# Optimization experiments

Hardware: AMD Instinct MI355X
Metric: run time of the kernel (lower is better)

The kernel has to match this reference:

```python
import jax, jax.numpy as jnp
import numpy as np

K_S = 7
PAD = 3

def _normalize(x, eps=1e-7):
    n = jnp.sqrt(jnp.sum(x * x, axis=-1, keepdims=True))
    return x / jnp.maximum(n, eps)

def _sample_early(feat, pid):
    # feat: [B,C,H,W]; gather fixed random patch ids shared across batch
    B, C, H, W = feat.shape
    fr = jnp.transpose(feat, (0, 2, 3, 1)).reshape(B, H * W, C)
    x = fr[:, pid, :].reshape(B * pid.shape[0], C)
    return _normalize(x)

def _qs_attn(feat, num_patches):
    B, C, H, W = feat.shape
    L = H * W
    fr = jnp.transpose(feat, (0, 2, 3, 1)).reshape(B, L, C)  # [B,L,C]
    # F.unfold(kernel=7, stride=1, padding=3): torch layout [B, C*49, L] (channel-major)
    pad = jnp.pad(feat, ((0, 0), (0, 0), (PAD, PAD), (PAD, PAD)))
    patches = jnp.stack([pad[:, :, i:i + H, j:j + W]
                         for i in range(K_S) for j in range(K_S)], axis=2)  # [B,C,49,H,W]
    feat_local = patches.reshape(B, C * K_S * K_S, L)
    # faithful to original: permute then reshape (B, L, k*k, C)
    feat_k_local = jnp.transpose(feat_local, (0, 2, 1)).reshape(B, L, K_S * K_S, C)
    # local attention: dots over window, softmax over the 49 window positions
    dots_local = jnp.einsum('blkc,blc->blk', feat_k_local, fr)
    attn_local = jax.nn.softmax(dots_local, axis=2)  # [B,L,49]
    logp = jnp.log(attn_local)
    prob = jnp.where(jnp.isinf(logp), 0.0, -logp)
    entropy = jnp.sum(attn_local * prob, axis=2)  # [B,L]
    idx = jnp.argsort(entropy, axis=1)[:, :num_patches]  # lowest-entropy patches [B,P]
    # global attention, only rows at selected patch ids (same math as slicing full BxLxL)
    q = jnp.take_along_axis(fr, idx[:, :, None], axis=1)  # [B,P,C]
    dots_global = jnp.einsum('bpc,blc->bpl', q, fr)
    attn_qs = jax.nn.softmax(dots_global, axis=2)  # [B,P,L]
    out = jnp.einsum('bpl,blc->bpc', attn_qs, fr)  # [B,P,C]
    return _normalize(out.reshape(B * num_patches, C))

def setup_inputs() -> dict:
    key = jax.random.key(0)
    k0, k1, k2, k3, k4, k5, k6 = jax.random.split(key, 7)
    return {
        'feat0': jax.random.normal(k0, (2, 64, 256, 256), dtype=jnp.float32),
        'feat1': jax.random.normal(k1, (2, 128, 128, 128), dtype=jnp.float32),
        'feat2': jax.random.normal(k2, (2, 256, 64, 64), dtype=jnp.float32),
        'feat3': jax.random.normal(k3, (2, 256, 64, 64), dtype=jnp.float32),
        'pid0': jax.random.randint(k4, (64,), 0, 256 * 256, dtype=jnp.int64)
                if jax.config.jax_enable_x64 else jax.random.randint(k4, (64,), 0, 256 * 256),
        'pid1': jax.random.randint(k5, (64,), 0, 128 * 128),
        'pid2': jax.random.randint(k6, (64,), 0, 64 * 64),
        'num_patches': 64,
    }

def reference(feat0, feat1, feat2, feat3, pid0, pid1, pid2, num_patches):
    x0 = _sample_early(feat0, pid0)
    x1 = _sample_early(feat1, pid1)
    x2 = _sample_early(feat2, pid2)
    x3 = _qs_attn(feat3, num_patches)
    return (x0, x1, x2, x3)
```

## Files before the change

kernel.cpp:

```cpp
#include <hip/hip_runtime.h>
#include <hip/hip_bf16.h>
#include <cstdint>
#include <cstddef>

__device__ __forceinline__ float wave_max_f(float v){
  #pragma unroll
  for (int m = 32; m; m >>= 1) v = fmaxf(v, __shfl_xor(v, m));
  return v;
}
__device__ __forceinline__ float wave_sum_f(float v){
  #pragma unroll
  for (int m = 32; m; m >>= 1) v += __shfl_xor(v, m);
  return v;
}
__device__ __forceinline__ int wave_sum_i(int v){
  #pragma unroll
  for (int m = 32; m; m >>= 1) v += __shfl_xor(v, m);
  return v;
}

#define C3   256
#define HW3  4096
#define NP   64

template<int C, int LOGHW>
__device__ __forceinline__ void sample_body(const float* __restrict__ feat,
                                            const int* __restrict__ pid,
                                            float* __restrict__ out,
                                            int r, int lane){
  const int b = r >> 6, p = r & 63;
  const int l = pid[p];
  const float* fb = feat + (((size_t)b * C) << LOGHW);
  constexpr int V = C / 64;
  float v[V];
  float sq = 0.f;
  #pragma unroll
  for (int i = 0; i < V; ++i){
    const int c = lane + 64 * i;
    v[i] = fb[(((size_t)c) << LOGHW) + l];
    sq += v[i] * v[i];
  }
  sq = wave_sum_f(sq);
  const float nrm = fmaxf(sqrtf(sq), 1e-7f);
  #pragma unroll
  for (int i = 0; i < V; ++i)
    out[(size_t)r * C + lane + 64 * i] = v[i] / nrm;
}

__global__ __launch_bounds__(1024, 8)
void ldots_kernel(const float* __restrict__ feat3, float* __restrict__ dotsl,
                  const float* __restrict__ f0, const float* __restrict__ f1,
                  const float* __restrict__ f2,
                  const int* __restrict__ p0, const int* __restrict__ p1,
                  const int* __restrict__ p2,
                  float* __restrict__ o0, float* __restrict__ o1,
                  float* __restrict__ o2){
  __shared__ float fr_sh[C3 * 64];
  const int raw = blockIdx.x;
  const int tid = threadIdx.x, wid = tid >> 6, lane = tid & 63;

  if (raw >= 512){
    const int sidx = ((raw - 512) << 4) | wid;
    const int g = sidx >> 7, r = sidx & 127;
    if (g == 0)      sample_body<64, 16>(f0, p0, o0, r, lane);
    else if (g == 1) sample_body<128, 14>(f1, p1, o1, r, lane);
    else             sample_body<256, 12>(f2, p2, o2, r, lane);
    return;
  }

  const int work = (raw & 7) * 64 + (raw >> 3);
  const int kg = work & 3;
  const int bh = work >> 2;
  const int b = bh >> 6, h = bh & 63;
  const int w = lane;
  const float* fb = feat3 + ((size_t)b << 20);

  {
    const int c2b = wid << 4;
    #pragma unroll
    for (int j = 0; j < 16; ++j){
      const int c2 = c2b + j;
      fr_sh[(c2 << 6) + w] = fb[((size_t)c2 << 12) + (h << 6) + w];
    }
  }
  __syncthreads();

  const int k2v = (wid << 2) | kg;
  if (k2v >= 49) return;
  const int k2 = __builtin_amdgcn_readfirstlane(k2v);
  const float* fr_w = fr_sh + w;
  const int f0i = k2 << 8;
  const int c0 = f0i / 49;
  const int k0 = f0i - c0 * 49;

  int   vof[7];
  float msk[7];
  #pragma unroll
  for (int kj = 0; kj < 7; ++kj){
    const int s = w + kj - 3;
    msk[kj] = ((unsigned)s < 64u) ? 1.f : 0.f;
    vof[kj] = s < 0 ? 0 : (s > 63 ? 63 : s);
  }

  float acc = 0.f;
  int c2 = 0;

  auto partial = [&](int c, int klo, int khi){
    for (int k = klo; k < khi; ++k){
      const int ki = k / 7, kj = k - (k / 7) * 7;
      const int hh = h + ki - 3;
      float wv = 0.f;
      if ((unsigned)hh < 64u){
        const int sw = w + kj - 3;
        const int swc = sw < 0 ? 0 : (sw > 63 ? 63 : sw);
        const float x = fb[((size_t)c << 12) + (hh << 6) + swc];
        wv = ((unsigned)sw < 64u) ? x : 0.f;
      }
      acc = fmaf(wv, fr_w[c2 << 6], acc);
      ++c2;
    }
  };

  partial(c0, k0, 49);

  #pragma unroll
  for (int j = 1; j <= 4; ++j){
    const int c = c0 + j;
    const float* chan = fb + ((size_t)c << 12);
    #pragma unroll
    for (int ki = 0; ki < 7; ++ki){
      const int hh = h + ki - 3;
      if ((unsigned)hh < 64u){
        const float* row = chan + (hh << 6);
        #pragma unroll
        for (int kj = 0; kj < 7; ++kj){
          const float x = row[vof[kj]];
          acc = fmaf(x * msk[kj], fr_w[(c2 + ki * 7 + kj) << 6], acc);
        }
      }
    }
    c2 += 49;
  }

  {
    const int rem = 11 + k0;
    const int khi = rem < 49 ? rem : 49;
    partial(c0 + 5, 0, khi);
    if (rem > 49) partial(c0 + 6, 0, rem - 49);
  }

  dotsl[(((size_t)(b * 49 + k2)) << 12) + (h << 6) + w] = acc;
}

__global__ __launch_bounds__(64)
void lent_kernel(const float* __restrict__ dotsl, float* __restrict__ ent){
  const int blk = blockIdx.x;
  const int b = blk >> 6;
  const int l = ((blk & 63) << 6) + threadIdx.x;
  const float* dl = dotsl + (((size_t)b * 49) << 12);
  float m = -INFINITY;
  #pragma unroll
  for (int k = 0; k < 49; ++k) m = fmaxf(m, dl[((size_t)k << 12) + l]);
  float s = 0.f, ts = 0.f;
  #pragma unroll
  for (int k = 0; k < 49; ++k){
    const float d = dl[((size_t)k << 12) + l] - m;
    const float e = expf(d);
    s += e; ts += e * d;
  }
  ent[b * HW3 + l] = logf(s) - ts / s;
}

__global__ __launch_bounds__(256)
void rank_select_kernel(const float* __restrict__ ent, int* __restrict__ idx){
  __shared__ unsigned long long keys[HW3];
  const int blk = blockIdx.x;
  const int b  = blk >> 6;
  const int cg = blk & 63;
  const int t = threadIdx.x, wid = t >> 6, lane = t & 63;
  for (int i = t; i < HW3; i += 256){
    const float e = ent[b * HW3 + i];
    unsigned u = __float_as_uint(e);
    u = (u & 0x80000000u) ? ~u : (u | 0x80000000u);
    keys[i] = ((unsigned long long)u << 32) | (unsigned)i;
  }
  __syncthreads();
  #pragma unroll
  for (int j = 0; j < 16; ++j){
    const int cand = (cg << 6) + (wid << 4) + j;
    const unsigned long long kc = keys[cand];
    int cnt = 0;
    #pragma unroll 8
    for (int i = lane; i < HW3; i += 64)
      cnt += (keys[i] < kc) ? 1 : 0;
    cnt = wave_sum_i(cnt);
    if (lane == 0 && cnt < NP) idx[b * NP + cnt] = cand;
  }
}

__global__ __launch_bounds__(256)
void gdots_kernel(const float* __restrict__ feat3, const int* __restrict__ idx,
                  float* __restrict__ dg, float* __restrict__ bmax){
  __shared__ float4 q_int[C3];
  __shared__ float red4[4][4];
  const int raw = blockIdx.x;
  const int work = (raw & 7) * 64 + (raw >> 3);
  const int bpg = work >> 4, lc = work & 15;
  const int b = bpg >> 4;
  const int bp0 = (b << 6) + ((bpg & 15) << 2);
  const int t = threadIdx.x, lane = t & 63, wid = t >> 6;
  const float* fb = feat3 + ((size_t)b << 20);
  {
    float4 qv;
    qv.x = fb[((size_t)t << 12) + idx[bp0 + 0]];
    qv.y = fb[((size_t)t << 12) + idx[bp0 + 1]];
    qv.z = fb[((size_t)t << 12) + idx[bp0 + 2]];
    qv.w = fb[((size_t)t << 12) + idx[bp0 + 3]];
    q_int[t] = qv;
  }
  __syncthreads();
  const int l = (lc << 8) + t;
  float a0 = 0.f, a1 = 0.f, a2 = 0.f, a3 = 0.f;
  #pragma unroll 8
  for (int c = 0; c < C3; ++c){
    const float fv = fb[((size_t)c << 12) + l];
    const float4 q = q_int[c];
    a0 = fmaf(fv, q.x, a0); a1 = fmaf(fv, q.y, a1);
    a2 = fmaf(fv, q.z, a2); a3 = fmaf(fv, q.w, a3);
  }
  dg[((size_t)(bp0 + 0) << 12) + l] = a0;
  dg[((size_t)(bp0 + 1) << 12) + l] = a1;
  dg[((size_t)(bp0 + 2) << 12) + l] = a2;
  dg[((size_t)(bp0 + 3) << 12) + l] = a3;
  const float m0 = wave_max_f(a0), m1 = wave_max_f(a1);
  const float m2 = wave_max_f(a2), m3 = wave_max_f(a3);
  if (lane == 0){
    red4[wid][0] = m0; red4[wid][1] = m1;
    red4[wid][2] = m2; red4[wid][3] = m3;
  }
  __syncthreads();
  if (t < 4){
    const float m = fmaxf(fmaxf(red4[0][t], red4[1][t]),
                          fmaxf(red4[2][t], red4[3][t]));
    bmax[(bp0 + t) * 16 + lc] = m;
  }
}

#define PSW(l) ((l) ^ (((l) >> 3) & 7))
__global__ __launch_bounds__(256)
void pv_kernel(const float* __restrict__ feat3, const float* __restrict__ dg,
               const float* __restrict__ bmax, float* __restrict__ outraw){
  __shared__ float4 p_int[HW3];
  float* red = reinterpret_cast<float*>(p_int);
  const int raw = blockIdx.x;
  const int work = (raw & 7) * 32 + (raw >> 3);
  const int bpg = work >> 3, cg = work & 7;
  const int b = bpg >> 4;
  const int bp0 = (b << 6) + ((bpg & 15) << 2);
  const int t = threadIdx.x, lane = t & 63, wid = t >> 6;
  const float* fb = feat3 + ((size_t)b << 20);

  float e_reg[4][16];
  float iq[4];
  #pragma unroll
  for (int q = 0; q < 4; ++q){
    const int bp = bp0 + q;
    float m = -INFINITY;
    #pragma unroll
    for (int i = 0; i < 16; ++i) m = fmaxf(m, bmax[bp * 16 + i]);
    float s = 0.f;
    #pragma unroll
    for (int i = 0; i < 16; ++i){
      const float e = expf(dg[((size_t)bp << 12) + (i << 8) + t] - m);
      e_reg[q][i] = e;
      s += e;
    }
    s = wave_sum_f(s);
    if (lane == 0) red[wid] = s;
    __syncthreads();
    const float stot = red[0] + red[1] + red[2] + red[3];
    __syncthreads();
    iq[q] = 1.f / stot;
  }

  #pragma unroll
  for (int i = 0; i < 16; ++i){
    const int l = (i << 8) + t;
    float4 pv;
    pv.x = e_reg[0][i] * iq[0];
    pv.y = e_reg[1][i] * iq[1];
    pv.z = e_reg[2][i] * iq[2];
    pv.w = e_reg[3][i] * iq[3];
    p_int[PSW(l)] = pv;
  }
  __syncthreads();
  float s[8][4];
  #pragma unroll
  for (int j = 0; j < 8; ++j)
    #pragma unroll
    for (int q = 0; q < 4; ++q) s[j][q] = 0.f;

  const int cbase = (cg << 5) + (wid << 3);
  for (int i = 0; i < 16; ++i){
    const int l4 = (i << 6) + lane;
    const float4 p0 = p_int[PSW(4 * l4 + 0)];
    const float4 p1 = p_int[PSW(4 * l4 + 1)];
    const float4 p2 = p_int[PSW(4 * l4 + 2)];
    const float4 p3 = p_int[PSW(4 * l4 + 3)];
    #pragma unroll
    for (int j = 0; j < 8; ++j){
      const float4 a = *reinterpret_cast<const float4*>(
          fb + (((size_t)(cbase + j)) << 12) + 4 * (size_t)l4);
      s[j][0] += a.x * p0.x + a.y * p1.x + a.z * p2.x + a.w * p3.x;
      s[j][1] += a.x * p0.y + a.y * p1.y + a.z * p2.y + a.w * p3.y;
      s[j][2] += a.x * p0.z + a.y * p1.z + a.z * p2.z + a.w * p3.z;
      s[j][3] += a.x * p0.w + a.y * p1.w + a.z * p2.w + a.w * p3.w;
    }
  }
  #pragma unroll
  for (int j = 0; j < 8; ++j){
    #pragma unroll
    for (int q = 0; q < 4; ++q){
      const float v = wave_sum_f(s[j][q]);
      if (lane == 0) outraw[(bp0 + q) * C3 + cbase + j] = v;
    }
  }
}

__global__ __launch_bounds__(256)
void norm_kernel(const float* __restrict__ outraw, float* __restrict__ out3){
  __shared__ float red[4];
  const int bp = blockIdx.x, t = threadIdx.x, lane = t & 63, wid = t >> 6;
  const float v = outraw[bp * C3 + t];
  const float sq = wave_sum_f(v * v);
  if (lane == 0) red[wid] = sq;
  __syncthreads();
  const float nrm = fmaxf(sqrtf(red[0] + red[1] + red[2] + red[3]), 1e-7f);
  out3[(size_t)bp * C3 + t] = v / nrm;
}

extern "C" void kernel_launch(void* const* d_in, const int* in_sizes, int n_in,
                              void* d_out, int out_size, void* d_ws, size_t ws_size,
                              hipStream_t stream){
  const float* feat0 = (const float*)d_in[0];
  const float* feat1 = (const float*)d_in[1];
  const float* feat2 = (const float*)d_in[2];
  const float* feat3 = (const float*)d_in[3];
  const int*   pid0  = (const int*)d_in[4];
  const int*   pid1  = (const int*)d_in[5];
  const int*   pid2  = (const int*)d_in[6];

  float* out  = (float*)d_out;
  float* out0 = out;
  float* out1 = out + 8192;
  float* out2 = out + 24576;
  float* out3 = out + 57344;

  float* ws       = (float*)d_ws;
  float* ent_ws   = ws;
  int*   idx_ws   = (int*)(ws + 8192);
  float* dotsl_ws = ws + 8320;
  float* dg_ws    = dotsl_ws + 401408;
  float* bmax_ws  = dg_ws + 524288;
  float* oraw_ws  = bmax_ws + 2048;

  ldots_kernel<<<536, 1024, 0, stream>>>(feat3, dotsl_ws,
                                         feat0, feat1, feat2,
                                         pid0, pid1, pid2,
                                         out0, out1, out2);
  lent_kernel<<<128, 64, 0, stream>>>(dotsl_ws, ent_ws);
  rank_select_kernel<<<128, 256, 0, stream>>>(ent_ws, idx_ws);
  gdots_kernel<<<512, 256, 0, stream>>>(feat3, idx_ws, dg_ws, bmax_ws);
  pv_kernel<<<256, 256, 0, stream>>>(feat3, dg_ws, bmax_ws, oraw_ws);
  norm_kernel<<<128, 256, 0, stream>>>(oraw_ws, out3);
}
```

Baseline: 98.57 us.

## Split PV over L into 8 slices with separate softmax-stats kernel

Softmax row max and inverse sum move into a new gsm_kernel. pv_kernel now splits the L dimension into 8 slices, so it launches 2048 blocks instead of 256, and each block builds only a small slice of probabilities in shared memory. Partial outputs are written per slice and summed in norm_kernel. This raises parallelism and lowers shared memory per block to improve occupancy, at the cost of one extra launch, recomputing exp across channel groups, and reusing workspace regions.

Measured after the change: 138.2 us. 40.2% more time.

```diff
diff --git a/kernel.cpp b/kernel.cpp
--- a/kernel.cpp
+++ b/kernel.cpp
@@ -246,54 +246,60 @@
   }
 }
 
-#define PSW(l) ((l) ^ (((l) >> 3) & 7))
 __global__ __launch_bounds__(256)
+void gsm_kernel(const float* __restrict__ dg, const float* __restrict__ bmax,
+                float* __restrict__ mrow, float* __restrict__ srow){
+  __shared__ float red[4];
+  const int bp = blockIdx.x, t = threadIdx.x, lane = t & 63, wid = t >> 6;
+  float m = -INFINITY;
+  #pragma unroll
+  for (int i = 0; i < 16; ++i) m = fmaxf(m, bmax[bp * 16 + i]);
+  float s = 0.f;
+  #pragma unroll
+  for (int i = 0; i < 16; ++i) s += expf(dg[((size_t)bp << 12) + (i << 8) + t] - m);
+  s = wave_sum_f(s);
+  if (lane == 0) red[wid] = s;
+  __syncthreads();
+  if (t == 0){
+    mrow[bp] = m;
+    srow[bp] = 1.f / (red[0] + red[1] + red[2] + red[3]);
+  }
+}
+
+__global__ __launch_bounds__(256, 6)
 void pv_kernel(const float* __restrict__ feat3, const float* __restrict__ dg,
-               const float* __restrict__ bmax, float* __restrict__ outraw){
-  __shared__ float4 p_int[HW3];
-  float* red = reinterpret_cast<float*>(p_int);
+               const float* __restrict__ mrow, const float* __restrict__ srow,
+               float* __restrict__ opart){
+  __shared__ float4 pp[4][130];
   const int raw = blockIdx.x;
-  const int work = (raw & 7) * 32 + (raw >> 3);
-  const int bpg = work >> 3, cg = work & 7;
-  const int b = bpg >> 4;
-  const int bp0 = (b << 6) + ((bpg & 15) << 2);
+  const int work = (raw & 7) * 256 + (raw >> 3);
+  const int pg = work & 15;
+  const int rest = work >> 4;
+  const int ls = rest & 7;
+  const int cg = (rest >> 3) & 7;
+  const int b  = rest >> 6;
+  const int bp0 = (b << 6) + (pg << 2);
   const int t = threadIdx.x, lane = t & 63, wid = t >> 6;
   const float* fb = feat3 + ((size_t)b << 20);
 
-  float e_reg[4][16];
-  float iq[4];
-  #pragma unroll
-  for (int q = 0; q < 4; ++q){
-    const int bp = bp0 + q;
-    float m = -INFINITY;
-    #pragma unroll
-    for (int i = 0; i < 16; ++i) m = fmaxf(m, bmax[bp * 16 + i]);
-    float s = 0.f;
-    #pragma unroll
-    for (int i = 0; i < 16; ++i){
-      const float e = expf(dg[((size_t)bp << 12) + (i << 8) + t] - m);
-      e_reg[q][i] = e;
-      s += e;
-    }
-    s = wave_sum_f(s);
-    if (lane == 0) red[wid] = s;
-    __syncthreads();
-    const float stot = red[0] + red[1] + red[2] + red[3];
-    __syncthreads();
-    iq[q] = 1.f / stot;
-  }
-
-  #pragma unroll
-  for (int i = 0; i < 16; ++i){
-    const int l = (i << 8) + t;
+  const float m0 = mrow[bp0 + 0], i0 = srow[bp0 + 0];
+  const float m1 = mrow[bp0 + 1], i1 = srow[bp0 + 1];
+  const float m2 = mrow[bp0 + 2], i2 = srow[bp0 + 2];
+  const float m3 = mrow[bp0 + 3], i3 = srow[bp0 + 3];
+
+  #pragma unroll
+  for (int rep = 0; rep < 2; ++rep){
+    const int lo = t + (rep << 8);
+    const int l = (ls << 9) + lo;
     float4 pv;
-    pv.x = e_reg[0][i] * iq[0];
-    pv.y = e_reg[1][i] * iq[1];
-    pv.z = e_reg[2][i] * iq[2];
-    pv.w = e_reg[3][i] * iq[3];
-    p_int[PSW(l)] = pv;
-  }
-  __syncthreads();
+    pv.x = expf(dg[((size_t)(bp0 + 0) << 12) + l] - m0) * i0;
+    pv.y = expf(dg[((size_t)(bp0 + 1) << 12) + l] - m1) * i1;
+    pv.z = expf(dg[((size_t)(bp0 + 2) << 12) + l] - m2) * i2;
+    pv.w = expf(dg[((size_t)(bp0 + 3) << 12) + l] - m3) * i3;
+    pp[lo & 3][lo >> 2] = pv;
+  }
+  __syncthreads();
+
   float s[8][4];
   #pragma unroll
   for (int j = 0; j < 8; ++j)
@@ -301,16 +307,17 @@
     for (int q = 0; q < 4; ++q) s[j][q] = 0.f;
 
   const int cbase = (cg << 5) + (wid << 3);
-  for (int i = 0; i < 16; ++i){
-    const int l4 = (i << 6) + lane;
-    const float4 p0 = p_int[PSW(4 * l4 + 0)];
-    const float4 p1 = p_int[PSW(4 * l4 + 1)];
-    const float4 p2 = p_int[PSW(4 * l4 + 2)];
-    const float4 p3 = p_int[PSW(4 * l4 + 3)];
+  #pragma unroll
+  for (int ii = 0; ii < 2; ++ii){
+    const int l4 = (ii << 6) + lane;
+    const float4 p0 = pp[0][l4];
+    const float4 p1 = pp[1][l4];
+    const float4 p2 = pp[2][l4];
+    const float4 p3 = pp[3][l4];
     #pragma unroll
     for (int j = 0; j < 8; ++j){
       const float4 a = *reinterpret_cast<const float4*>(
-          fb + (((size_t)(cbase + j)) << 12) + 4 * (size_t)l4);
+          fb + (((size_t)(cbase + j)) << 12) + (ls << 9) + 4 * (size_t)l4);
       s[j][0] += a.x * p0.x + a.y * p1.x + a.z * p2.x + a.w * p3.x;
       s[j][1] += a.x * p0.y + a.y * p1.y + a.z * p2.y + a.w * p3.y;
       s[j][2] += a.x * p0.z + a.y * p1.z + a.z * p2.z + a.w * p3.z;
@@ -322,16 +329,20 @@
     #pragma unroll
     for (int q = 0; q < 4; ++q){
       const float v = wave_sum_f(s[j][q]);
-      if (lane == 0) outraw[(bp0 + q) * C3 + cbase + j] = v;
+      if (lane == 0)
+        opart[((((bp0 + q) << 8) | (cbase + j)) << 3) | ls] = v;
     }
   }
 }
 
 __global__ __launch_bounds__(256)
-void norm_kernel(const float* __restrict__ outraw, float* __restrict__ out3){
+void norm_kernel(const float* __restrict__ opart, float* __restrict__ out3){
   __shared__ float red[4];
   const int bp = blockIdx.x, t = threadIdx.x, lane = t & 63, wid = t >> 6;
-  const float v = outraw[bp * C3 + t];
+  const float* op = opart + (((size_t)(bp << 8) | t) << 3);
+  float v = 0.f;
+  #pragma unroll
+  for (int ls = 0; ls < 8; ++ls) v += op[ls];
   const float sq = wave_sum_f(v * v);
   if (lane == 0) red[wid] = sq;
   __syncthreads();
@@ -362,7 +373,9 @@
   float* dotsl_ws = ws + 8320;
   float* dg_ws    = dotsl_ws + 401408;
   float* bmax_ws  = dg_ws + 524288;
-  float* oraw_ws  = bmax_ws + 2048;
+  float* mrow_ws  = ent_ws;
+  float* srow_ws  = ent_ws + 128;
+  float* opart_ws = dotsl_ws;
 
   ldots_kernel<<<536, 1024, 0, stream>>>(feat3, dotsl_ws,
                                          feat0, feat1, feat2,
@@ -371,6 +384,7 @@
   lent_kernel<<<128, 64, 0, stream>>>(dotsl_ws, ent_ws);
   rank_select_kernel<<<128, 256, 0, stream>>>(ent_ws, idx_ws);
   gdots_kernel<<<512, 256, 0, stream>>>(feat3, idx_ws, dg_ws, bmax_ws);
-  pv_kernel<<<256, 256, 0, stream>>>(feat3, dg_ws, bmax_ws, oraw_ws);
-  norm_kernel<<<128, 256, 0, stream>>>(oraw_ws, out3);
-}
+  gsm_kernel<<<128, 256, 0, stream>>>(dg_ws, bmax_ws, mrow_ws, srow_ws);
+  pv_kernel<<<2048, 256, 0, stream>>>(feat3, dg_ws, mrow_ws, srow_ws, opart_ws);
+  norm_kernel<<<128, 256, 0, stream>>>(opart_ws, out3);
+}
```

## Split softmax normalization into separate kernel and read probabilities from global in PV

Applied to the files above, without the earlier changes.

Moves the softmax exp/normalize of the global attention rows out of pv_kernel into a new pfill_kernel that writes normalized probabilities back in place. Each pv block previously recomputed the softmax for its 4 rows, redundantly across 8 channel groups, then staged the result in 64KB of LDS. Now pv_kernel reads probabilities directly from global/L2 with no LDS, which permits higher occupancy (launch bounds 6) and a work order grouping channel groups. This adds an extra kernel launch and a global round trip for the probabilities.

After: 125.4 us. 1.27x slower.

```diff
diff --git a/kernel.cpp b/kernel.cpp
--- a/kernel.cpp
+++ b/kernel.cpp
@@ -246,83 +246,75 @@
   }
 }
 
-#define PSW(l) ((l) ^ (((l) >> 3) & 7))
 __global__ __launch_bounds__(256)
-void pv_kernel(const float* __restrict__ feat3, const float* __restrict__ dg,
-               const float* __restrict__ bmax, float* __restrict__ outraw){
-  __shared__ float4 p_int[HW3];
-  float* red = reinterpret_cast<float*>(p_int);
+void pfill_kernel(float* __restrict__ dg, const float* __restrict__ bmax){
+  __shared__ float red[4];
+  const int bp = blockIdx.x, t = threadIdx.x, lane = t & 63, wid = t >> 6;
+  float m = -INFINITY;
+  #pragma unroll
+  for (int i = 0; i < 16; ++i) m = fmaxf(m, bmax[bp * 16 + i]);
+  float e[16];
+  float s = 0.f;
+  #pragma unroll
+  for (int i = 0; i < 16; ++i){
+    e[i] = expf(dg[((size_t)bp << 12) + (i << 8) + t] - m);
+    s += e[i];
+  }
+  s = wave_sum_f(s);
+  if (lane == 0) red[wid] = s;
+  __syncthreads();
+  const float inv = 1.f / (red[0] + red[1] + red[2] + red[3]);
+  #pragma unroll
+  for (int i = 0; i < 16; ++i)
+    dg[((size_t)bp << 12) + (i << 8) + t] = e[i] * inv;
+}
+
+__global__ __launch_bounds__(256, 6)
+void pv_kernel(const float* __restrict__ feat3, const float* __restrict__ p,
+               float* __restrict__ outraw){
   const int raw = blockIdx.x;
   const int work = (raw & 7) * 32 + (raw >> 3);
-  const int bpg = work >> 3, cg = work & 7;
-  const int b = bpg >> 4;
-  const int bp0 = (b << 6) + ((bpg & 15) << 2);
+  const int cg = work >> 5;
+  const int rest = work & 31;
+  const int b = rest >> 4, pg = rest & 15;
+  const int bp0 = (b << 6) + (pg << 2);
   const int t = threadIdx.x, lane = t & 63, wid = t >> 6;
   const float* fb = feat3 + ((size_t)b << 20);
-
-  float e_reg[4][16];
-  float iq[4];
-  #pragma unroll
-  for (int q = 0; q < 4; ++q){
-    const int bp = bp0 + q;
-    float m = -INFINITY;
-    #pragma unroll
-    for (int i = 0; i < 16; ++i) m = fmaxf(m, bmax[bp * 16 + i]);
-    float s = 0.f;
-    #pragma unroll
-    for (int i = 0; i < 16; ++i){
-      const float e = expf(dg[((size_t)bp << 12) + (i << 8) + t] - m);
-      e_reg[q][i] = e;
-      s += e;
-    }
-    s = wave_sum_f(s);
-    if (lane == 0) red[wid] = s;
-    __syncthreads();
-    const float stot = red[0] + red[1] + red[2] + red[3];
-    __syncthreads();
-    iq[q] = 1.f / stot;
-  }
-
-  #pragma unroll
-  for (int i = 0; i < 16; ++i){
-    const int l = (i << 8) + t;
-    float4 pv;
-    pv.x = e_reg[0][i] * iq[0];
-    pv.y = e_reg[1][i] * iq[1];
-    pv.z = e_reg[2][i] * iq[2];
-    pv.w = e_reg[3][i] * iq[3];
-    p_int[PSW(l)] = pv;
-  }
-  __syncthreads();
-  float s[8][4];
+  const int c0 = (cg << 5) + (wid << 3);
+
+  const float4* p0 = reinterpret_cast<const float4*>(p + ((size_t)(bp0 + 0) << 12));
+  const float4* p1 = reinterpret_cast<const float4*>(p + ((size_t)(bp0 + 1) << 12));
+  const float4* p2 = reinterpret_cast<const float4*>(p + ((size_t)(bp0 + 2) << 12));
+  const float4* p3 = reinterpret_cast<const float4*>(p + ((size_t)(bp0 + 3) << 12));
+
+  float acc[8][4];
   #pragma unroll
   for (int j = 0; j < 8; ++j)
     #pragma unroll
-    for (int q = 0; q < 4; ++q) s[j][q] = 0.f;
-
-  const int cbase = (cg << 5) + (wid << 3);
-  for (int i = 0; i < 16; ++i){
-    const int l4 = (i << 6) + lane;
-    const float4 p0 = p_int[PSW(4 * l4 + 0)];
-    const float4 p1 = p_int[PSW(4 * l4 + 1)];
-    const float4 p2 = p_int[PSW(4 * l4 + 2)];
-    const float4 p3 = p_int[PSW(4 * l4 + 3)];
+    for (int q = 0; q < 4; ++q) acc[j][q] = 0.f;
+
+  for (int ii = 0; ii < 16; ++ii){
+    const int l4 = (ii << 6) + lane;
+    const float4 q0 = p0[l4];
+    const float4 q1 = p1[l4];
+    const float4 q2 = p2[l4];
+    const float4 q3 = p3[l4];
     #pragma unroll
     for (int j = 0; j < 8; ++j){
       const float4 a = *reinterpret_cast<const float4*>(
-          fb + (((size_t)(cbase + j)) << 12) + 4 * (size_t)l4);
-      s[j][0] += a.x * p0.x + a.y * p1.x + a.z * p2.x + a.w * p3.x;
-      s[j][1] += a.x * p0.y + a.y * p1.y + a.z * p2.y + a.w * p3.y;
-      s[j][2] += a.x * p0.z + a.y * p1.z + a.z * p2.z + a.w * p3.z;
-      s[j][3] += a.x * p0.w + a.y * p1.w + a.z * p2.w + a.w * p3.w;
+          fb + (((size_t)(c0 + j)) << 12) + 4 * (size_t)l4);
+      acc[j][0] += a.x * q0.x + a.y * q0.y + a.z * q0.z + a.w * q0.w;
+      acc[j][1] += a.x * q1.x + a.y * q1.y + a.z * q1.z + a.w * q1.w;
+      acc[j][2] += a.x * q2.x + a.y * q2.y + a.z * q2.z + a.w * q2.w;
+      acc[j][3] += a.x * q3.x + a.y * q3.y + a.z * q3.z + a.w * q3.w;
     }
   }
   #pragma unroll
   for (int j = 0; j < 8; ++j){
     #pragma unroll
     for (int q = 0; q < 4; ++q){
-      const float v = wave_sum_f(s[j][q]);
-      if (lane == 0) outraw[(bp0 + q) * C3 + cbase + j] = v;
+      const float v = wave_sum_f(acc[j][q]);
+      if (lane == 0) outraw[(bp0 + q) * C3 + c0 + j] = v;
     }
   }
 }
@@ -371,6 +363,7 @@
   lent_kernel<<<128, 64, 0, stream>>>(dotsl_ws, ent_ws);
   rank_select_kernel<<<128, 256, 0, stream>>>(ent_ws, idx_ws);
   gdots_kernel<<<512, 256, 0, stream>>>(feat3, idx_ws, dg_ws, bmax_ws);
-  pv_kernel<<<256, 256, 0, stream>>>(feat3, dg_ws, bmax_ws, oraw_ws);
+  pfill_kernel<<<128, 256, 0, stream>>>(dg_ws, bmax_ws);
+  pv_kernel<<<256, 256, 0, stream>>>(feat3, dg_ws, oraw_ws);
   norm_kernel<<<128, 256, 0, stream>>>(oraw_ws, out3);
 }
```
